# Kernel optimization log

Hardware: AMD Instinct MI355X
Metric: run time of the kernel (lower is better)

Reference implementation:

```python
import jax, jax.numpy as jnp
import numpy as np

N_NODES = 100000
N_EDGES = 1600000
NUM_GRAPHS = 4096
HID = 128
F_IN = 11
F_OUT = 19


def setup_inputs() -> dict:
    key = jax.random.key(0)
    ks = jax.random.split(key, 8)
    x = jax.random.normal(ks[0], (N_NODES, F_IN), dtype=jnp.float32)
    edge_src = jax.random.randint(ks[1], (N_EDGES,), 0, N_NODES)
    edge_dst = jax.random.randint(ks[2], (N_EDGES,), 0, N_NODES)
    batch = jnp.sort(jax.random.randint(ks[3], (N_NODES,), 0, NUM_GRAPHS))
    W1 = jax.random.normal(ks[4], (F_IN, HID), dtype=jnp.float32) / np.sqrt(F_IN)
    b1 = jnp.zeros((HID,), dtype=jnp.float32)
    W2 = jax.random.normal(ks[5], (HID, HID), dtype=jnp.float32) / np.sqrt(HID)
    b2 = jnp.zeros((HID,), dtype=jnp.float32)
    Wlin = jax.random.normal(ks[6], (HID, F_OUT), dtype=jnp.float32) / np.sqrt(HID)
    blin = jnp.zeros((F_OUT,), dtype=jnp.float32)
    return {"x": x, "edge_src": edge_src, "edge_dst": edge_dst, "batch": batch,
            "W1": W1, "b1": b1, "W2": W2, "b2": b2, "Wlin": Wlin, "blin": blin}


def _gcn_conv(x, W, b, src, dst, norm, n_nodes):
    # x: [N, Fin] -> h: [N, Fout]; gather-normalize-scatter over edges (self-loops included in src/dst/norm)
    h = x @ W
    msgs = h[src] * norm[:, None]              # [E+N, Fout]
    out = jax.ops.segment_sum(msgs, dst, num_segments=n_nodes)
    return out + b


def reference(x, edge_src, edge_dst, batch, W1, b1, W2, b2, Wlin, blin):
    n = x.shape[0]
    # add self-loops (GCNConv default)
    loops = jnp.arange(n)
    src = jnp.concatenate([edge_src, loops])
    dst = jnp.concatenate([edge_dst, loops])
    # symmetric normalization deg^-1/2[src] * deg^-1/2[dst], deg computed on dst with self-loops
    deg = jax.ops.segment_sum(jnp.ones_like(dst, dtype=x.dtype), dst, num_segments=n)
    dinv = jnp.where(deg > 0, jax.lax.rsqrt(deg), 0.0)
    norm = dinv[src] * dinv[dst]
    h = _gcn_conv(x, W1, b1, src, dst, norm, n)
    h = jax.nn.relu(h)
    h = _gcn_conv(h, W2, b2, src, dst, norm, n)
    # global mean pool over batch assignment
    sums = jax.ops.segment_sum(h, batch, num_segments=NUM_GRAPHS)
    cnts = jax.ops.segment_sum(jnp.ones((n,), dtype=h.dtype), batch, num_segments=NUM_GRAPHS)
    pooled = sums / jnp.maximum(cnts, 1.0)[:, None]   # [NUM_GRAPHS, HID]
    return pooled @ Wlin + blin                       # [NUM_GRAPHS, F_OUT]
```

## Files before the change

### kernel.cpp

```cpp
#include <hip/hip_runtime.h>
#include <hip/hip_fp16.h>

#define N_NODES 100000
#define N_EDGES 1600000
#define NUM_G   4096
#define HID     128
#define F_IN    11
#define F_PAD   16
#define F_OUT   19

#define NB      256
#define KPB     391
#define BCAP    8192
#define GCAP    1024
#define P01_EPB 2048
#define NREG    8
#define REGW    12500
#define GPB     4
#define NAGG    782

__device__ inline void acc_row_f16(float* acc, uint4 u, float w) {
    const __half2* hp = (const __half2*)&u;
#pragma unroll
    for (int i = 0; i < 4; ++i) {
        acc[2 * i]     += __half2float(__low2half(hp[i]))  * w;
        acc[2 * i + 1] += __half2float(__high2half(hp[i])) * w;
    }
}
__device__ inline void add_row_f16(float* acc, uint4 u) {
    const __half2* hp = (const __half2*)&u;
#pragma unroll
    for (int i = 0; i < 4; ++i) {
        acc[2 * i]     += __half2float(__low2half(hp[i]));
        acc[2 * i + 1] += __half2float(__high2half(hp[i]));
    }
}

__global__ void p1_place(const int* __restrict__ src, const int* __restrict__ dst,
                         int* __restrict__ bcur, unsigned int* __restrict__ ebuf) {
    __shared__ int h[NB];
    __shared__ int base[NB];
    h[threadIdx.x] = 0;
    __syncthreads();
    unsigned int pk[8]; int bn[8];
    int b0 = blockIdx.x * P01_EPB;
    int e8 = b0 + threadIdx.x * 8;
    if (e8 + 8 <= N_EDGES) {
        int4 s0 = *(const int4*)(src + e8);
        int4 s1 = *(const int4*)(src + e8 + 4);
        int4 d0 = *(const int4*)(dst + e8);
        int4 d1 = *(const int4*)(dst + e8 + 4);
        int ss[8] = { s0.x, s0.y, s0.z, s0.w, s1.x, s1.y, s1.z, s1.w };
        int dd[8] = { d0.x, d0.y, d0.z, d0.w, d1.x, d1.y, d1.z, d1.w };
#pragma unroll
        for (int k = 0; k < 8; ++k) {
            bn[k] = dd[k] / KPB;
            pk[k] = ((unsigned)ss[k] << 9) | (unsigned)(dd[k] - bn[k] * KPB);
        }
    } else {
#pragma unroll
        for (int k = 0; k < 8; ++k) {
            int e = e8 + k;
            if (e < N_EDGES) {
                int d = dst[e];
                bn[k] = d / KPB;
                pk[k] = ((unsigned)src[e] << 9) | (unsigned)(d - bn[k] * KPB);
            } else bn[k] = -1;
        }
    }
#pragma unroll
    for (int k = 0; k < 8; ++k)
        if (bn[k] >= 0) atomicAdd(&h[bn[k]], 1);
    __syncthreads();
    {
        int c = h[threadIdx.x];
        base[threadIdx.x] = c ? atomicAdd(&bcur[threadIdx.x], c) : 0;
    }
    __syncthreads();
    h[threadIdx.x] = 0;
    __syncthreads();
#pragma unroll
    for (int k = 0; k < 8; ++k) {
        if (bn[k] >= 0) {
            int r = atomicAdd(&h[bn[k]], 1);
            ebuf[(size_t)bn[k] * BCAP + base[bn[k]] + r] = pk[k];
        }
    }
}

__global__ void p2_build(const unsigned int* __restrict__ ebuf, const int* __restrict__ bcur,
                         const float* __restrict__ x,
                         int* __restrict__ row_ptr, int* __restrict__ deg,
                         int* __restrict__ col, float* __restrict__ wd,
                         float* __restrict__ dinv, __half* __restrict__ xp) {
    __shared__ int hist[512];
    __shared__ float ldinv[512];
    __shared__ int wsum[8];
    __shared__ int woff[8];
    int b  = blockIdx.x;
    int t  = threadIdx.x;
    int dbase = b * KPB;
    int nd = N_NODES - dbase; if (nd > KPB) nd = KPB;
    hist[t] = 0;
    __syncthreads();
    int e0 = b * BCAP;
    int e1 = e0 + bcur[b];
    for (int e = e0 + t; e < e1; e += 512)
        atomicAdd(&hist[ebuf[e] & 511u], 1);
    __syncthreads();
    int v = hist[t];
    int lane = t & 63, wv = t >> 6;
    int sv = v;
#pragma unroll
    for (int off = 1; off < 64; off <<= 1) {
        int n = __shfl_up(sv, off, 64);
        if (lane >= off) sv += n;
    }
    if (lane == 63) wsum[wv] = sv;
    __syncthreads();
    if (t == 0) {
        int run = 0;
#pragma unroll
        for (int w = 0; w < 8; ++w) { woff[w] = run; run += wsum[w]; }
    }
    __syncthreads();
    int excl = sv - v + woff[wv];
    float di = rsqrtf(1.0f + (float)v);
    ldinv[t] = di;
    if (t < nd) {
        row_ptr[dbase + t] = e0 + excl;
        deg[dbase + t]     = v;
        dinv[dbase + t]    = di;
    }
    __syncthreads();
    hist[t] = e0 + excl;
    __syncthreads();
    for (int e = e0 + t; e < e1; e += 512) {
        unsigned int w = ebuf[e];
        int dl = (int)(w & 511u);
        int pos = atomicAdd(&hist[dl], 1);
        col[pos] = (int)(w >> 9);
        wd[pos]  = ldinv[dl];
    }
    for (int idx = t; idx < nd * F_PAD; idx += 512) {
        int vl = idx >> 4, f = idx & 15;
        int gv = dbase + vl;
        xp[(size_t)gv * F_PAD + f] =
            __float2half_rn((f < F_IN) ? ldinv[vl] * x[(size_t)gv * F_IN + f] : 0.f);
    }
}

__global__ void agg_es8(const __half* __restrict__ xp, const int* __restrict__ row_ptr,
                        const int* __restrict__ deg, const int* __restrict__ col,
                        const float* __restrict__ dinv,
                        const float* __restrict__ W1, const float* __restrict__ b1,
                        __half* __restrict__ Bh,
                        const int* __restrict__ batch, const float* __restrict__ wd,
                        uint2* __restrict__ ewp, int* __restrict__ gro,
                        int* __restrict__ gb) {
    __shared__ float xs[128][F_PAD];
    __shared__ float W1s[F_IN * HID];
    __shared__ float b1s[HID];
    __shared__ float ds[128];
    __shared__ int cnt[NREG];
    __shared__ int cur[NREG];
    __shared__ int range[2];
    int tid = threadIdx.x;

    if (blockIdx.x < NAGG) {
        for (int i = tid; i < F_IN * HID; i += 256) W1s[i] = W1[i];
        if (tid < HID) b1s[tid] = b1[tid];
        const uint4* xp4 = (const uint4*)xp;
        int v0   = blockIdx.x * 128;
        int v    = v0 + (tid >> 1);
        int lane = tid & 1;
        if (v < N_NODES) {
            if (lane == 0) ds[tid >> 1] = dinv[v];
            float a[8];
#pragma unroll
            for (int k = 0; k < 8; ++k) a[k] = 0.f;
            add_row_f16(a, xp4[(size_t)v * 2 + lane]);
            int j = row_ptr[v], end = j + deg[v];
            for (; j + 3 < end; j += 4) {
                int s0 = col[j], s1 = col[j + 1], s2 = col[j + 2], s3 = col[j + 3];
                uint4 u0 = xp4[(size_t)s0 * 2 + lane];
                uint4 u1 = xp4[(size_t)s1 * 2 + lane];
                uint4 u2 = xp4[(size_t)s2 * 2 + lane];
                uint4 u3 = xp4[(size_t)s3 * 2 + lane];
                add_row_f16(a, u0); add_row_f16(a, u1);
                add_row_f16(a, u2); add_row_f16(a, u3);
            }
            for (; j < end; ++j)
                add_row_f16(a, xp4[(size_t)col[j] * 2 + lane]);
#pragma unroll
            for (int k = 0; k < 8; ++k) xs[tid >> 1][lane * 8 + k] = a[k];
        }
        __syncthreads();
        int jf   = tid & 127;
        int half = tid >> 7;
        int nmax = N_NODES - v0; if (nmax > 128) nmax = 128;
        for (int n = half; n < nmax; n += 2) {
            float a = 0.f;
#pragma unroll
            for (int k = 0; k < F_IN; ++k) a += xs[n][k] * W1s[k * HID + jf];
            float dv = ds[n];
            float h = fmaxf(dv * a + b1s[jf], 0.f);
            Bh[(size_t)(v0 + n) * HID + jf] = __float2half_rn(dv * h);
        }
    } else {
        int g = blockIdx.x - NAGG;
        if (tid < NREG) cnt[tid] = 0;
        if (tid < 2) {
            int tgt = g + tid;
            int lo = 0, hi = N_NODES;
            while (lo < hi) { int m = (lo + hi) >> 1; if (batch[m] < tgt) lo = m + 1; else hi = m; }
            range[tid] = lo;
        }
        __syncthreads();
        int r0 = range[0], r1 = range[1];
        if (tid == 0) {
            gb[g] = r0;
            if (g == NUM_G - 1) gb[NUM_G] = N_NODES;
        }
        int bb0 = 0, bb1 = -1;
        if (r1 > r0) { bb0 = r0 / KPB; bb1 = (r1 - 1) / KPB; }
        for (int bb = bb0; bb <= bb1; ++bb) {
            int vlo = r0 > bb * KPB ? r0 : bb * KPB;
            int vhi = r1 < bb * KPB + KPB ? r1 : bb * KPB + KPB;
            int ee0 = row_ptr[vlo];
            int ee1 = row_ptr[vhi - 1] + deg[vhi - 1];
            for (int e = ee0 + tid; e < ee1; e += 256)
                atomicAdd(&cnt[(unsigned)col[e] / REGW], 1);
        }
        for (int v = r0 + tid; v < r1; v += 256)
            atomicAdd(&cnt[(unsigned)v / REGW], 1);
        __syncthreads();
        if (tid == 0) {
            int run = g * GCAP;
#pragma unroll
            for (int p = 0; p < NREG; ++p) {
                gro[g * 9 + p] = run;
                cur[p] = run;
                run += cnt[p];
            }
            gro[g * 9 + 8] = run;
        }
        __syncthreads();
        for (int bb = bb0; bb <= bb1; ++bb) {
            int vlo = r0 > bb * KPB ? r0 : bb * KPB;
            int vhi = r1 < bb * KPB + KPB ? r1 : bb * KPB + KPB;
            int ee0 = row_ptr[vlo];
            int ee1 = row_ptr[vhi - 1] + deg[vhi - 1];
            for (int e = ee0 + tid; e < ee1; e += 256) {
                int s = col[e];
                int pos = atomicAdd(&cur[(unsigned)s / REGW], 1);
                ewp[pos] = make_uint2((unsigned)s, __float_as_uint(wd[e]));
            }
        }
        for (int v = r0 + tid; v < r1; v += 256) {
            int pos = atomicAdd(&cur[(unsigned)v / REGW], 1);
            ewp[pos] = make_uint2((unsigned)v, __float_as_uint(dinv[v]));
        }
    }
}

__global__ void pool_gather(const __half* __restrict__ Bh,
                            const int* __restrict__ gro,
                            const uint2* __restrict__ ewp,
                            float* __restrict__ part) {
    __shared__ float red[32][HID + 4];
    int b    = blockIdx.x;
    int gset = b >> 3;
    int p    = b & 7;
    int tid  = threadIdx.x;
    int grp  = tid >> 3;
    int lane = tid & 7;
    int g    = gset * GPB + (grp >> 3);
    int q    = grp & 7;
    const uint4* B4 = (const uint4*)Bh;
    float acc[16];
#pragma unroll
    for (int k = 0; k < 16; ++k) acc[k] = 0.f;

    int e0 = gro[g * 9 + p], e1 = gro[g * 9 + p + 1];
    int e = e0 + q;
    for (; e + 8 < e1; e += 16) {
        uint2 q0 = ewp[e], q1 = ewp[e + 8];
        uint4 u00 = B4[(size_t)q0.x * 16 + lane * 2];
        uint4 u01 = B4[(size_t)q0.x * 16 + lane * 2 + 1];
        uint4 u10 = B4[(size_t)q1.x * 16 + lane * 2];
        uint4 u11 = B4[(size_t)q1.x * 16 + lane * 2 + 1];
        float w0 = __uint_as_float(q0.y), w1 = __uint_as_float(q1.y);
        acc_row_f16(acc,     u00, w0);
        acc_row_f16(acc + 8, u01, w0);
        acc_row_f16(acc,     u10, w1);
        acc_row_f16(acc + 8, u11, w1);
    }
    for (; e < e1; e += 8) {
        uint2 q0 = ewp[e];
        uint4 u00 = B4[(size_t)q0.x * 16 + lane * 2];
        uint4 u01 = B4[(size_t)q0.x * 16 + lane * 2 + 1];
        float w0 = __uint_as_float(q0.y);
        acc_row_f16(acc,     u00, w0);
        acc_row_f16(acc + 8, u01, w0);
    }
#pragma unroll
    for (int k = 0; k < 16; ++k) red[grp][lane * 16 + k] = acc[k];
    __syncthreads();
    for (int i = tid; i < GPB * HID; i += 256) {
        int gg = i >> 7, f = i & 127;
        int rb = gg * 8;
        float s = 0.f;
#pragma unroll
        for (int r = 0; r < 8; ++r) s += red[rb + r][f];
        part[(size_t)((gset * GPB + gg) * NREG + p) * HID + f] = s;
    }
}

__global__ void combine_head(const float* __restrict__ part, const int* __restrict__ gb,
                             const float* __restrict__ W2, const float* __restrict__ b2,
                             const float* __restrict__ Wlin, const float* __restrict__ blin,
                             float* __restrict__ out) {
    __shared__ float r[HID];
    __shared__ float tt[HID];
    int g = blockIdx.x;
    int f = threadIdx.x;
    float s = 0.f;
#pragma unroll
    for (int p = 0; p < NREG; ++p) s += part[(size_t)(g * NREG + p) * HID + f];
    int cnt = gb[g + 1] - gb[g];
    float inv = (cnt > 0) ? 1.0f / (float)cnt : 0.f;
    r[f] = s * inv;
    __syncthreads();
    float bs = (cnt > 0) ? 1.0f : 0.f;
    float tj = b2[f] * bs;
#pragma unroll 8
    for (int k = 0; k < HID; ++k) tj += r[k] * W2[k * HID + f];
    tt[f] = tj;
    __syncthreads();
    if (f < F_OUT) {
        float o = blin[f];
#pragma unroll 8
        for (int k = 0; k < HID; ++k) o += tt[k] * Wlin[k * F_OUT + f];
        out[(size_t)g * F_OUT + f] = o;
    }
}

extern "C" void kernel_launch(void* const* d_in, const int* in_sizes, int n_in,
                              void* d_out, int out_size, void* d_ws, size_t ws_size,
                              hipStream_t stream) {
    const float* x    = (const float*)d_in[0];
    const int*   esrc = (const int*)  d_in[1];
    const int*   edst = (const int*)  d_in[2];
    const int*   batch= (const int*)  d_in[3];
    const float* W1   = (const float*)d_in[4];
    const float* b1   = (const float*)d_in[5];
    const float* W2   = (const float*)d_in[6];
    const float* b2   = (const float*)d_in[7];
    const float* Wlin = (const float*)d_in[8];
    const float* blin = (const float*)d_in[9];
    float* out = (float*)d_out;

    char* p = (char*)d_ws;
    float*        dinv    = (float*)p;        p += sizeof(float) * N_NODES;
    __half*       xp      = (__half*)p;       p += sizeof(__half) * (size_t)N_NODES * F_PAD;
    __half*       Bh      = (__half*)p;       p += sizeof(__half) * (size_t)N_NODES * HID;
    unsigned int* ebuf    = (unsigned int*)p; p += sizeof(unsigned int) * (size_t)NB * BCAP;
    int*          col     = (int*)p;          p += sizeof(int) * (size_t)NB * BCAP;
    float*        wd      = (float*)p;        p += sizeof(float) * (size_t)NB * BCAP;
    int*          deg     = (int*)p;          p += sizeof(int) * N_NODES;
    uint2*        ewp     = (uint2*)p;        p += sizeof(uint2) * (size_t)NUM_G * GCAP;
    float*        part    = (float*)p;        p += sizeof(float) * (size_t)NUM_G * NREG * HID;
    int*          row_ptr = (int*)p;          p += sizeof(int) * (N_NODES + 4);
    int*          gb      = (int*)p;          p += sizeof(int) * (NUM_G + 4);
    int*          gro     = (int*)p;          p += sizeof(int) * (NUM_G * 9 + 4);
    int*          bcur    = (int*)p;          p += sizeof(int) * NB;

    const int nblk_e = (N_EDGES + P01_EPB - 1) / P01_EPB;

    hipMemsetAsync(bcur, 0, sizeof(int) * NB, stream);
    p1_place<<<nblk_e, 256, 0, stream>>>(esrc, edst, bcur, ebuf);
    p2_build<<<NB, 512, 0, stream>>>(ebuf, bcur, x, row_ptr, deg, col, wd, dinv, xp);

    agg_es8<<<NAGG + NUM_G, 256, 0, stream>>>(xp, row_ptr, deg, col, dinv, W1, b1, Bh,
                                              batch, wd, ewp, gro, gb);

    pool_gather<<<(NUM_G / GPB) * NREG, 256, 0, stream>>>(Bh, gro, ewp, part);

    combine_head<<<NUM_G, HID, 0, stream>>>(part, gb, W2, b2, Wlin, blin, out);
}
```

Before: 235.0 us.

## Split agg rows across 4 lanes and batch 8 graphs per combine_head block

The first-layer gather now gives 4 threads to each node, with 8-byte loads and an 8-way unrolled neighbour loop. Blocks cover 64 nodes, so there are twice as many aggregation blocks. This aims to put more independent gathers in flight and improve latency hiding. Separately, combine_head now handles 8 graphs per 256-thread block, and each thread accumulates 4 graphs so every W2 load is reused across them. This cuts global W2 traffic and the number of launched blocks, at the cost of more repeated W1 loading across the extra agg blocks.

```diff
diff --git a/kernel.cpp b/kernel.cpp
--- a/kernel.cpp
+++ b/kernel.cpp
@@ -17,7 +17,8 @@
 #define NREG    8
 #define REGW    12500
 #define GPB     4
-#define NAGG    782
+#define NAGG    1563
+#define CH_G    8
 
 __device__ inline void acc_row_f16(float* acc, uint4 u, float w) {
     const __half2* hp = (const __half2*)&u;
@@ -27,13 +28,12 @@
         acc[2 * i + 1] += __half2float(__high2half(hp[i])) * w;
     }
 }
-__device__ inline void add_row_f16(float* acc, uint4 u) {
+__device__ inline void add_row_f16_u2(float* acc, uint2 u) {
     const __half2* hp = (const __half2*)&u;
-#pragma unroll
-    for (int i = 0; i < 4; ++i) {
-        acc[2 * i]     += __half2float(__low2half(hp[i]));
-        acc[2 * i + 1] += __half2float(__high2half(hp[i]));
-    }
+    acc[0] += __half2float(__low2half(hp[0]));
+    acc[1] += __half2float(__high2half(hp[0]));
+    acc[2] += __half2float(__low2half(hp[1]));
+    acc[3] += __half2float(__high2half(hp[1]));
 }
 
 __global__ void p1_place(const int* __restrict__ src, const int* __restrict__ dst,
@@ -158,10 +158,10 @@
                         const int* __restrict__ batch, const float* __restrict__ wd,
                         uint2* __restrict__ ewp, int* __restrict__ gro,
                         int* __restrict__ gb) {
-    __shared__ float xs[128][F_PAD];
+    __shared__ float xs[64][F_PAD];
     __shared__ float W1s[F_IN * HID];
     __shared__ float b1s[HID];
-    __shared__ float ds[128];
+    __shared__ float ds[64];
     __shared__ int cnt[NREG];
     __shared__ int cur[NREG];
     __shared__ int range[2];
@@ -170,35 +170,51 @@
     if (blockIdx.x < NAGG) {
         for (int i = tid; i < F_IN * HID; i += 256) W1s[i] = W1[i];
         if (tid < HID) b1s[tid] = b1[tid];
-        const uint4* xp4 = (const uint4*)xp;
-        int v0   = blockIdx.x * 128;
-        int v    = v0 + (tid >> 1);
-        int lane = tid & 1;
+        const uint2* xp2 = (const uint2*)xp;
+        int v0   = blockIdx.x * 64;
+        int v    = v0 + (tid >> 2);
+        int lane = tid & 3;
         if (v < N_NODES) {
-            if (lane == 0) ds[tid >> 1] = dinv[v];
-            float a[8];
-#pragma unroll
-            for (int k = 0; k < 8; ++k) a[k] = 0.f;
-            add_row_f16(a, xp4[(size_t)v * 2 + lane]);
+            if (lane == 0) ds[tid >> 2] = dinv[v];
+            float a[4];
+#pragma unroll
+            for (int k = 0; k < 4; ++k) a[k] = 0.f;
+            add_row_f16_u2(a, xp2[(size_t)v * 4 + lane]);
             int j = row_ptr[v], end = j + deg[v];
+            for (; j + 7 < end; j += 8) {
+                int s0 = col[j],     s1 = col[j + 1], s2 = col[j + 2], s3 = col[j + 3];
+                int s4 = col[j + 4], s5 = col[j + 5], s6 = col[j + 6], s7 = col[j + 7];
+                uint2 u0 = xp2[(size_t)s0 * 4 + lane];
+                uint2 u1 = xp2[(size_t)s1 * 4 + lane];
+                uint2 u2 = xp2[(size_t)s2 * 4 + lane];
+                uint2 u3 = xp2[(size_t)s3 * 4 + lane];
+                uint2 u4 = xp2[(size_t)s4 * 4 + lane];
+                uint2 u5 = xp2[(size_t)s5 * 4 + lane];
+                uint2 u6 = xp2[(size_t)s6 * 4 + lane];
+                uint2 u7 = xp2[(size_t)s7 * 4 + lane];
+                add_row_f16_u2(a, u0); add_row_f16_u2(a, u1);
+                add_row_f16_u2(a, u2); add_row_f16_u2(a, u3);
+                add_row_f16_u2(a, u4); add_row_f16_u2(a, u5);
+                add_row_f16_u2(a, u6); add_row_f16_u2(a, u7);
+            }
             for (; j + 3 < end; j += 4) {
                 int s0 = col[j], s1 = col[j + 1], s2 = col[j + 2], s3 = col[j + 3];
-                uint4 u0 = xp4[(size_t)s0 * 2 + lane];
-                uint4 u1 = xp4[(size_t)s1 * 2 + lane];
-                uint4 u2 = xp4[(size_t)s2 * 2 + lane];
-                uint4 u3 = xp4[(size_t)s3 * 2 + lane];
-                add_row_f16(a, u0); add_row_f16(a, u1);
-                add_row_f16(a, u2); add_row_f16(a, u3);
+                uint2 u0 = xp2[(size_t)s0 * 4 + lane];
+                uint2 u1 = xp2[(size_t)s1 * 4 + lane];
+                uint2 u2 = xp2[(size_t)s2 * 4 + lane];
+                uint2 u3 = xp2[(size_t)s3 * 4 + lane];
+                add_row_f16_u2(a, u0); add_row_f16_u2(a, u1);
+                add_row_f16_u2(a, u2); add_row_f16_u2(a, u3);
             }
             for (; j < end; ++j)
-                add_row_f16(a, xp4[(size_t)col[j] * 2 + lane]);
-#pragma unroll
-            for (int k = 0; k < 8; ++k) xs[tid >> 1][lane * 8 + k] = a[k];
+                add_row_f16_u2(a, xp2[(size_t)col[j] * 4 + lane]);
+#pragma unroll
+            for (int k = 0; k < 4; ++k) xs[tid >> 2][lane * 4 + k] = a[k];
         }
         __syncthreads();
         int jf   = tid & 127;
         int half = tid >> 7;
-        int nmax = N_NODES - v0; if (nmax > 128) nmax = 128;
+        int nmax = N_NODES - v0; if (nmax > 64) nmax = 64;
         for (int n = half; n < nmax; n += 2) {
             float a = 0.f;
 #pragma unroll
@@ -321,28 +337,52 @@
                              const float* __restrict__ W2, const float* __restrict__ b2,
                              const float* __restrict__ Wlin, const float* __restrict__ blin,
                              float* __restrict__ out) {
-    __shared__ float r[HID];
-    __shared__ float tt[HID];
-    int g = blockIdx.x;
-    int f = threadIdx.x;
-    float s = 0.f;
-#pragma unroll
-    for (int p = 0; p < NREG; ++p) s += part[(size_t)(g * NREG + p) * HID + f];
-    int cnt = gb[g + 1] - gb[g];
-    float inv = (cnt > 0) ? 1.0f / (float)cnt : 0.f;
-    r[f] = s * inv;
-    __syncthreads();
-    float bs = (cnt > 0) ? 1.0f : 0.f;
-    float tj = b2[f] * bs;
+    __shared__ float r[CH_G][HID];
+    __shared__ float tt[CH_G][HID + 4];
+    __shared__ float bsc[CH_G];
+    int g0  = blockIdx.x * CH_G;
+    int tid = threadIdx.x;
+    int f   = tid & 127;
+    int gh  = tid >> 7;
+    int q0  = gh * 4;
+#pragma unroll
+    for (int c = 0; c < 4; ++c) {
+        int gg = q0 + c;
+        int g  = g0 + gg;
+        float s = 0.f;
+#pragma unroll
+        for (int p = 0; p < NREG; ++p) s += part[(size_t)(g * NREG + p) * HID + f];
+        int cnt = gb[g + 1] - gb[g];
+        float inv = (cnt > 0) ? 1.0f / (float)cnt : 0.f;
+        r[gg][f] = s * inv;
+        if (f == 0) bsc[gg] = (cnt > 0) ? 1.0f : 0.f;
+    }
+    __syncthreads();
+    float bf = b2[f];
+    float t0 = bf * bsc[q0];
+    float t1 = bf * bsc[q0 + 1];
+    float t2 = bf * bsc[q0 + 2];
+    float t3 = bf * bsc[q0 + 3];
+#pragma unroll 4
+    for (int k = 0; k < HID; ++k) {
+        float w = W2[k * HID + f];
+        t0 += r[q0][k] * w;
+        t1 += r[q0 + 1][k] * w;
+        t2 += r[q0 + 2][k] * w;
+        t3 += r[q0 + 3][k] * w;
+    }
+    tt[q0][f]     = t0;
+    tt[q0 + 1][f] = t1;
+    tt[q0 + 2][f] = t2;
+    tt[q0 + 3][f] = t3;
+    __syncthreads();
+    if (tid < CH_G * F_OUT) {
+        int gg = tid / F_OUT;
+        int fo = tid - gg * F_OUT;
+        float o = blin[fo];
 #pragma unroll 8
-    for (int k = 0; k < HID; ++k) tj += r[k] * W2[k * HID + f];
-    tt[f] = tj;
-    __syncthreads();
-    if (f < F_OUT) {
-        float o = blin[f];
-#pragma unroll 8
-        for (int k = 0; k < HID; ++k) o += tt[k] * Wlin[k * F_OUT + f];
-        out[(size_t)g * F_OUT + f] = o;
+        for (int k = 0; k < HID; ++k) o += tt[gg][k] * Wlin[k * F_OUT + fo];
+        out[(size_t)(g0 + gg) * F_OUT + fo] = o;
     }
 }
 
@@ -387,5 +427,5 @@
 
     pool_gather<<<(NUM_G / GPB) * NREG, 256, 0, stream>>>(Bh, gro, ewp, part);
 
-    combine_head<<<NUM_G, HID, 0, stream>>>(part, gb, W2, b2, Wlin, blin, out);
-}
+    combine_head<<<NUM_G / CH_G, 256, 0, stream>>>(part, gb, W2, b2, Wlin, blin, out);
+}
```

After: 237.9 us. No clear change (+1.2%).
